# Kernel tuning notes

Measured on AMD Instinct MI355X. Metric: run time of the kernel, lower is better.

The kernel has to match this reference:

```python
import jax, jax.numpy as jnp
import numpy as np

B, M, D, E, K, T = 8192, 6, 128, 5, 2, 60
SHARED_W, UNSHARED_W, LB_W = 0.3, 0.7, 0.01

def _gelu(x):
    return jax.nn.gelu(x, approximate=False)

def _mlp3(x, w1, b1, w2, b2, w3, b3):
    h = _gelu(x @ w1 + b1)
    h = _gelu(h @ w2 + b2)
    return h @ w3 + b3

def _expert_stack(x, w1, b1, w2, b2, w3, b3):
    # x: [N, D]; weights stacked over experts e -> grouped GEMMs
    h = _gelu(jnp.einsum('nd,edh->enh', x, w1) + b1[:, None, :])
    h = _gelu(jnp.einsum('enh,ehg->eng', h, w2) + b2[:, None, :])
    return jnp.einsum('eng,ego->eno', h, w3) + b3[:, None, :]

def setup_inputs():
    key = jax.random.key(0)
    ks = iter(jax.random.split(key, 64))
    p = lambda shape, s=0.05: s * jax.random.normal(next(ks), shape, dtype=jnp.float32)
    return {
        'mode_features': jax.random.normal(next(ks), (B, M, D), dtype=jnp.float32),
        'rw1': p((D, 256)), 'rb1': p((256,)), 'rw2': p((256, 128)), 'rb2': p((128,)),
        'rw3': p((128, E)), 'rb3': p((E,)),
        'sh_tw1': p((D, 256)), 'sh_tb1': p((256,)), 'sh_tw2': p((256, 256)), 'sh_tb2': p((256,)),
        'sh_tw3': p((256, T * 2)), 'sh_tb3': p((T * 2,)),
        'sh_sw1': p((D, 128)), 'sh_sb1': p((128,)), 'sh_sw2': p((128, 64)), 'sh_sb2': p((64,)),
        'sh_sw3': p((64, 1)), 'sh_sb3': p((1,)),
        'ex_tw1': p((E, D, 256)), 'ex_tb1': p((E, 256)), 'ex_tw2': p((E, 256, 256)), 'ex_tb2': p((E, 256)),
        'ex_tw3': p((E, 256, T * 2)), 'ex_tb3': p((E, T * 2)),
        'ex_sw1': p((E, D, 128)), 'ex_sb1': p((E, 128)), 'ex_sw2': p((E, 128, 64)), 'ex_sb2': p((E, 64)),
        'ex_sw3': p((E, 64, 1)), 'ex_sb3': p((E, 1)),
    }

def reference(mode_features, rw1, rb1, rw2, rb2, rw3, rb3,
              sh_tw1, sh_tb1, sh_tw2, sh_tb2, sh_tw3, sh_tb3,
              sh_sw1, sh_sb1, sh_sw2, sh_sb2, sh_sw3, sh_sb3,
              ex_tw1, ex_tb1, ex_tw2, ex_tb2, ex_tw3, ex_tb3,
              ex_sw1, ex_sb1, ex_sw2, ex_sb2, ex_sw3, ex_sb3):
    b, m, d = mode_features.shape
    x = mode_features.reshape(b * m, d)
    # router (Dropout is identity in eval mode)
    logits = _mlp3(x, rw1, rb1, rw2, rb2, rw3, rb3)                 # [N, E]
    probs = jax.nn.softmax(logits, axis=-1)
    router_logits = logits.reshape(b, m, E)
    topk_logits, topk_idx = jax.lax.top_k(router_logits, K)         # [B, M, K]
    topk_probs = jax.nn.softmax(topk_logits, axis=-1)
    # shared expert on all tokens
    shared_traj = _mlp3(x, sh_tw1, sh_tb1, sh_tw2, sh_tb2, sh_tw3, sh_tb3).reshape(b, m, T, 2)
    shared_score = _mlp3(x, sh_sw1, sh_sb1, sh_sw2, sh_sb2, sh_sw3, sh_sb3).reshape(b, m)
    # all unshared experts computed densely (torch code also computes these for expert_predictions)
    traj_all = _expert_stack(x, ex_tw1, ex_tb1, ex_tw2, ex_tb2, ex_tw3, ex_tb3).reshape(E, b, m, T, 2)
    score_all = _expert_stack(x, ex_sw1, ex_sb1, ex_sw2, ex_sb2, ex_sw3, ex_sb3).reshape(E, b, m)
    # top-k combine: gather selected expert outputs (same math as the torch dispatch + index_add_)
    traj_bme = jnp.transpose(traj_all, (1, 2, 0, 3, 4))             # [B, M, E, T, 2]
    score_bme = jnp.transpose(score_all, (1, 2, 0))                 # [B, M, E]
    idx5 = jnp.broadcast_to(topk_idx[..., None, None], (b, m, K, T, 2))
    sel_traj = jnp.take_along_axis(traj_bme, idx5, axis=2)          # [B, M, K, T, 2]
    sel_score = jnp.take_along_axis(score_bme, topk_idx, axis=2)    # [B, M, K]
    unshared_traj = jnp.einsum('bmktc,bmk->bmtc', sel_traj, topk_probs)
    unshared_score = jnp.sum(sel_score * topk_probs, axis=-1)
    final_traj = SHARED_W * shared_traj + UNSHARED_W * unshared_traj
    final_score = SHARED_W * shared_score + UNSHARED_W * unshared_score
    # load-balance aux loss
    avg_probs = jnp.mean(probs, axis=0)                             # [E]
    entropy = -jnp.sum(avg_probs * jnp.log(avg_probs + 1e-8))
    l2 = jnp.mean((avg_probs - 1.0 / E) ** 2)
    aux_loss = -entropy * LB_W + 0.01 * l2
    return (final_traj, final_score, router_logits, topk_idx, aux_loss, traj_all, score_all)
```

## Files before the change

### kernel.cpp

```cpp
#include <hip/hip_runtime.h>
#include <hip/hip_bf16.h>
#include <cstdint>
#include <cstddef>

static constexpr int N_TOK = 49152;
static constexpr size_t OFF_TRAJ     = 0;
static constexpr size_t OFF_SCORE    = 5898240;
static constexpr size_t OFF_LOGITS   = 5947392;
static constexpr size_t OFF_IDX      = 6193152;
static constexpr size_t OFF_AUX      = 6291456;
static constexpr size_t OFF_TRAJALL  = 6291457;
static constexpr size_t OFF_SCOREALL = 35782657;

typedef short s16x8 __attribute__((ext_vector_type(8)));
typedef float f32x4 __attribute__((ext_vector_type(4)));
typedef f32x4 f32x4u __attribute__((aligned(4)));
typedef unsigned int u32;
typedef unsigned short u16;

static constexpr u32 O_T1 = 0,      O_T2 = 196608, O_T3 = 589824;
static constexpr u32 O_S1 = 774144, O_S2 = 872448;
static constexpr u32 OB_T1 = 0, OB_T2 = 1536, OB_T3 = 3072, OB_S1 = 3792, OB_S2 = 4560;
static constexpr u32 OW_S3 = 4944, OB_S3 = 5328;

__device__ __forceinline__ float gelu_exact(float x) {
    return 0.5f * x * (1.0f + erff(x * 0.70710678118654752440f));
}
__device__ __forceinline__ float gelu_f(float x) {
    const float x2 = x * x;
    const float u  = x * fmaf(0.07135486172f, x2, 1.5957691216057308f);
    const float t  = __expf(-u);
    return x * __builtin_amdgcn_rcpf(1.0f + t);
}
__device__ __forceinline__ float bf2f(u16 u) {
    return __uint_as_float(((u32)u) << 16);
}
__device__ __forceinline__ u16 f2bf(float v) {
    return ((__hip_bfloat16_raw)__float2bfloat16(v)).x;
}
__device__ __forceinline__ void gload16(const u16* g, u16* l) {
    __builtin_amdgcn_global_load_lds(
        (const __attribute__((address_space(1))) u32*)g,
        (__attribute__((address_space(3))) u32*)l, 16, 0, 0);
}
#define MFMA16(a, b, c) __builtin_amdgcn_mfma_f32_16x16x32_bf16(a, b, c, 0, 0, 0)
#define SBAR() __builtin_amdgcn_sched_barrier(0)

__device__ __forceinline__ s16x8 lds_frag(const u16* buf, int RBu16, int r, int c) {
    return *(const s16x8*)&buf[r * RBu16 + ((c ^ (r & 7)) << 3)];
}
__device__ __forceinline__ void lds_store4(u16* buf, int RBu16, int r, int colb,
                                           float v0, float v1, float v2, float v3) {
    const int ch = (colb >> 3) ^ (r & 7);
    ushort4 st = { f2bf(v0), f2bf(v1), f2bf(v2), f2bf(v3) };
    *(ushort4*)&buf[r * RBu16 + ch * 8 + (colb & 7)] = st;
}

template<bool GELU>
__global__ __launch_bounds__(256)
void mlp_gemm(const float* __restrict__ A, const float* __restrict__ W,
              const float* __restrict__ bias, float* __restrict__ C,
              int Kd, int H)
{
    __shared__ float As[32][128];
    __shared__ float Ws[32][132];

    const int tid  = threadIdx.x;
    const int tx   = tid & 15;
    const int ty   = tid >> 4;
    const int row0 = blockIdx.x * 128;
    const int col0 = blockIdx.y * 128;
    const int lm = tid >> 1;
    const int lk = (tid & 1) * 16;

    float acc[8][8] = {};

    for (int k0 = 0; k0 < Kd; k0 += 32) {
        {
            const float* src = A + (size_t)(row0 + lm) * Kd + k0 + lk;
            #pragma unroll
            for (int q = 0; q < 4; ++q) {
                float4 f = *(const float4*)(src + q * 4);
                As[lk + q * 4 + 0][lm] = f.x;
                As[lk + q * 4 + 1][lm] = f.y;
                As[lk + q * 4 + 2][lm] = f.z;
                As[lk + q * 4 + 3][lm] = f.w;
            }
        }
        {
            #pragma unroll
            for (int q = 0; q < 2; ++q) {
                const float* wsrc = W + (size_t)(k0 + ty + q * 16) * H + col0 + tx * 8;
                float4 g0 = *(const float4*)wsrc;
                float4 g1 = *(const float4*)(wsrc + 4);
                *(float4*)&Ws[ty + q * 16][tx * 8]     = g0;
                *(float4*)&Ws[ty + q * 16][tx * 8 + 4] = g1;
            }
        }
        __syncthreads();
        #pragma unroll
        for (int kk = 0; kk < 32; ++kk) {
            float a[8], w[8];
            *(float4*)&a[0] = *(const float4*)&As[kk][ty * 8];
            *(float4*)&a[4] = *(const float4*)&As[kk][ty * 8 + 4];
            *(float4*)&w[0] = *(const float4*)&Ws[kk][tx * 8];
            *(float4*)&w[4] = *(const float4*)&Ws[kk][tx * 8 + 4];
            #pragma unroll
            for (int i = 0; i < 8; ++i)
                #pragma unroll
                for (int j = 0; j < 8; ++j)
                    acc[i][j] = fmaf(a[i], w[j], acc[i][j]);
        }
        __syncthreads();
    }

    #pragma unroll
    for (int i = 0; i < 8; ++i) {
        const int r = row0 + ty * 8 + i;
        #pragma unroll
        for (int j = 0; j < 8; ++j) {
            const int c = col0 + tx * 8 + j;
            float v = acc[i][j] + bias[c];
            if (GELU) v = gelu_exact(v);
            C[(size_t)r * H + c] = v;
        }
    }
}

__global__ __launch_bounds__(256)
void router_l3post(const float* __restrict__ rh2, const float* __restrict__ w3,
                   const float* __restrict__ b3, float* __restrict__ logits,
                   float* __restrict__ oidx, float* __restrict__ tp,
                   int* __restrict__ ti, float* __restrict__ part)
{
    __shared__ float w3s[640];
    __shared__ float red[256];
    const int tid = threadIdx.x;
    for (int i = tid; i < 640; i += 256) w3s[i] = w3[i];
    __syncthreads();

    const int n = blockIdx.x * 256 + tid;
    const float* h = rh2 + (size_t)n * 128;

    float l[5];
    #pragma unroll
    for (int e = 0; e < 5; ++e) l[e] = b3[e];
    for (int k = 0; k < 128; k += 4) {
        float4 hv = *(const float4*)(h + k);
        #pragma unroll
        for (int e = 0; e < 5; ++e) {
            l[e] = fmaf(hv.x, w3s[(k + 0) * 5 + e], l[e]);
            l[e] = fmaf(hv.y, w3s[(k + 1) * 5 + e], l[e]);
            l[e] = fmaf(hv.z, w3s[(k + 2) * 5 + e], l[e]);
            l[e] = fmaf(hv.w, w3s[(k + 3) * 5 + e], l[e]);
        }
    }
    #pragma unroll
    for (int e = 0; e < 5; ++e) logits[(size_t)n * 5 + e] = l[e];

    float m = l[0];
    #pragma unroll
    for (int e = 1; e < 5; ++e) m = fmaxf(m, l[e]);
    float p[5], s = 0.f;
    #pragma unroll
    for (int e = 0; e < 5; ++e) { p[e] = expf(l[e] - m); s += p[e]; }
    const float inv = 1.0f / s;

    #pragma unroll
    for (int e = 0; e < 5; ++e) {
        red[tid] = p[e] * inv;
        __syncthreads();
        for (int off = 128; off > 0; off >>= 1) {
            if (tid < off) red[tid] += red[tid + off];
            __syncthreads();
        }
        if (tid == 0) part[blockIdx.x * 5 + e] = red[0];
        __syncthreads();
    }

    int i0 = 0; float v0 = l[0];
    #pragma unroll
    for (int e = 1; e < 5; ++e) if (l[e] > v0) { v0 = l[e]; i0 = e; }
    int i1 = -1; float v1 = -1e30f;
    #pragma unroll
    for (int e = 0; e < 5; ++e) if (e != i0 && l[e] > v1) { v1 = l[e]; i1 = e; }

    const float t  = expf(v1 - v0);
    const float q0 = 1.0f / (1.0f + t);
    const float q1 = t / (1.0f + t);

    oidx[(size_t)n * 2]     = (float)i0;
    oidx[(size_t)n * 2 + 1] = (float)i1;
    tp[n * 2] = q0; tp[n * 2 + 1] = q1;
    ti[n * 2] = i0; ti[n * 2 + 1] = i1;
}

__global__ __launch_bounds__(256)
void aux_kernel(const float* __restrict__ part, float* __restrict__ aux)
{
    __shared__ float avg[5];
    const int tid = threadIdx.x;
    if (tid < 5) {
        float s = 0.f;
        for (int b = 0; b < 192; ++b) s += part[b * 5 + tid];
        avg[tid] = s / (float)N_TOK;
    }
    __syncthreads();
    if (tid == 0) {
        float ent = 0.f, l2 = 0.f;
        #pragma unroll
        for (int e = 0; e < 5; ++e) {
            ent -= avg[e] * logf(avg[e] + 1e-8f);
            float d = avg[e] - 0.2f;
            l2 += d * d;
        }
        l2 *= (1.0f / 5.0f);
        aux[0] = -ent * 0.01f + 0.01f * l2;
    }
}

__global__ __launch_bounds__(512, 2)
void expert_fused(const u16* __restrict__ xb, const u16* __restrict__ wtb,
                  const float* __restrict__ biasp, float* __restrict__ out,
                  float* __restrict__ shtraj, float* __restrict__ shscore)
{
    __shared__ u16 xs[64 * 128];
    __shared__ u16 hb[64 * 256];
    float* hbf = (float*)hb;
    u16* s1p = hb;
    u16* s2p = hb + 64 * 128;

    const int tid  = threadIdx.x;
    const int lane = tid & 63;
    const int wave = tid >> 6;
    const int row0 = blockIdx.x * 64;
    const int e    = blockIdx.y;
    const int frow = lane & 15;
    const int kgrp = lane >> 4;
    const int c0   = wave * 32;

    #pragma unroll
    for (int i = 0; i < 2; ++i) {
        const int idx = i * 512 + tid;
        const int r = idx >> 4, c = idx & 15;
        gload16(xb + (size_t)(row0 + r) * 128 + ((c ^ (r & 7)) << 3), &xs[idx * 8]);
    }

    const int col3 = wave * 16 + kgrp * 4;
    const int r3   = (wave * 16 + frow) < 120 ? (wave * 16 + frow) : 119;

    s16x8 wf1[4][2];
    {
        const u16* w1p = wtb + O_T1 + e * 32768;
        #pragma unroll
        for (int n = 0; n < 2; ++n) {
            const u16* p = w1p + (size_t)(c0 + n * 16 + frow) * 128 + kgrp * 8;
            #pragma unroll
            for (int ks = 0; ks < 4; ++ks) wf1[ks][n] = *(const s16x8*)(p + ks * 32);
        }
    }
    SBAR();

    __syncthreads();

    f32x4 acc1[4][2] = {};
    #pragma unroll
    for (int ks = 0; ks < 4; ++ks)
        #pragma unroll
        for (int m = 0; m < 4; ++m) {
            const s16x8 a = lds_frag(xs, 128, m * 16 + frow, ks * 4 + kgrp);
            #pragma unroll
            for (int n = 0; n < 2; ++n)
                acc1[m][n] = MFMA16(wf1[ks][n], a, acc1[m][n]);
        }

    const u16* w2p = wtb + O_T2 + e * 65536;
    s16x8 wf2a[4][2];
    f32x4 bb1[2];
    #pragma unroll
    for (int n = 0; n < 2; ++n) {
        const u16* p = w2p + (size_t)(c0 + n * 16 + frow) * 256 + kgrp * 8;
        #pragma unroll
        for (int ks = 0; ks < 4; ++ks) wf2a[ks][n] = *(const s16x8*)(p + ks * 32);
        bb1[n] = *(const f32x4*)&biasp[OB_T1 + e * 256 + c0 + n * 16 + kgrp * 4];
    }
    SBAR();

    {
        #pragma unroll
        for (int n = 0; n < 2; ++n) {
            const int colb = c0 + n * 16 + kgrp * 4;
            #pragma unroll
            for (int m = 0; m < 4; ++m)
                lds_store4(hb, 256, m * 16 + frow, colb,
                           gelu_f(acc1[m][n][0] + bb1[n][0]),
                           gelu_f(acc1[m][n][1] + bb1[n][1]),
                           gelu_f(acc1[m][n][2] + bb1[n][2]),
                           gelu_f(acc1[m][n][3] + bb1[n][3]));
        }
    }
    __syncthreads();

    s16x8 wf2b[4][2];
    #pragma unroll
    for (int n = 0; n < 2; ++n) {
        const u16* p = w2p + (size_t)(c0 + n * 16 + frow) * 256 + 128 + kgrp * 8;
        #pragma unroll
        for (int ks = 0; ks < 4; ++ks) wf2b[ks][n] = *(const s16x8*)(p + ks * 32);
    }
    SBAR();

    f32x4 acc2[4][2] = {};
    #pragma unroll
    for (int ks = 0; ks < 4; ++ks)
        #pragma unroll
        for (int m = 0; m < 4; ++m) {
            const s16x8 a = lds_frag(hb, 256, m * 16 + frow, ks * 4 + kgrp);
            #pragma unroll
            for (int n = 0; n < 2; ++n)
                acc2[m][n] = MFMA16(wf2a[ks][n], a, acc2[m][n]);
        }
    #pragma unroll
    for (int ks = 0; ks < 4; ++ks)
        #pragma unroll
        for (int m = 0; m < 4; ++m) {
            const s16x8 a = lds_frag(hb, 256, m * 16 + frow, (ks + 4) * 4 + kgrp);
            #pragma unroll
            for (int n = 0; n < 2; ++n)
                acc2[m][n] = MFMA16(wf2b[ks][n], a, acc2[m][n]);
        }

    s16x8 wf3[8];
    f32x4 bb2[2];
    {
        const u16* w3p = wtb + O_T3 + e * 30720 + (size_t)r3 * 256 + kgrp * 8;
        #pragma unroll
        for (int ks = 0; ks < 8; ++ks) wf3[ks] = *(const s16x8*)(w3p + ks * 32);
        #pragma unroll
        for (int n = 0; n < 2; ++n)
            bb2[n] = *(const f32x4*)&biasp[OB_T2 + e * 256 + c0 + n * 16 + kgrp * 4];
    }
    SBAR();
    __syncthreads();

    {
        #pragma unroll
        for (int n = 0; n < 2; ++n) {
            const int colb = c0 + n * 16 + kgrp * 4;
            #pragma unroll
            for (int m = 0; m < 4; ++m)
                lds_store4(hb, 256, m * 16 + frow, colb,
                           gelu_f(acc2[m][n][0] + bb2[n][0]),
                           gelu_f(acc2[m][n][1] + bb2[n][1]),
                           gelu_f(acc2[m][n][2] + bb2[n][2]),
                           gelu_f(acc2[m][n][3] + bb2[n][3]));
        }
    }
    __syncthreads();

    s16x8 wfs1[4];
    f32x4 bb3 = *(const f32x4u*)&biasp[OB_T3 + e * 120 + (col3 < 120 ? col3 : 116)];
    {
        const u16* p = wtb + O_S1 + e * 16384 + (size_t)(wave * 16 + frow) * 128 + kgrp * 8;
        #pragma unroll
        for (int ks = 0; ks < 4; ++ks) wfs1[ks] = *(const s16x8*)(p + ks * 32);
    }
    SBAR();

    f32x4 acc3[4] = {};
    #pragma unroll
    for (int ks = 0; ks < 8; ++ks)
        #pragma unroll
        for (int m = 0; m < 4; ++m) {
            const s16x8 a = lds_frag(hb, 256, m * 16 + frow, ks * 4 + kgrp);
            acc3[m] = MFMA16(wf3[ks], a, acc3[m]);
        }
    __syncthreads();

    f32x4 accs1[4] = {};
    #pragma unroll
    for (int ks = 0; ks < 4; ++ks)
        #pragma unroll
        for (int m = 0; m < 4; ++m) {
            const s16x8 a = lds_frag(xs, 128, m * 16 + frow, ks * 4 + kgrp);
            accs1[m] = MFMA16(wfs1[ks], a, accs1[m]);
        }
    s16x8 wfs2[4];
    f32x4 bbs1;
    {
        const u16* p = wtb + O_S2 + e * 8192 + (size_t)((wave & 3) * 16 + frow) * 128 + kgrp * 8;
        #pragma unroll
        for (int ks = 0; ks < 4; ++ks) wfs2[ks] = *(const s16x8*)(p + ks * 32);
        bbs1 = *(const f32x4*)&biasp[OB_S1 + e * 128 + wave * 16 + kgrp * 4];
    }
    SBAR();
    {
        const int colb = wave * 16 + kgrp * 4;
        #pragma unroll
        for (int m = 0; m < 4; ++m)
            lds_store4(s1p, 128, m * 16 + frow, colb,
                       gelu_f(accs1[m][0] + bbs1[0]),
                       gelu_f(accs1[m][1] + bbs1[1]),
                       gelu_f(accs1[m][2] + bbs1[2]),
                       gelu_f(accs1[m][3] + bbs1[3]));
    }
    __syncthreads();

    if (wave < 4) {
        f32x4 accs2[4] = {};
        #pragma unroll
        for (int ks = 0; ks < 4; ++ks)
            #pragma unroll
            for (int m = 0; m < 4; ++m) {
                const s16x8 a = lds_frag(s1p, 128, m * 16 + frow, ks * 4 + kgrp);
                accs2[m] = MFMA16(wfs2[ks], a, accs2[m]);
            }
        const int colb = wave * 16 + kgrp * 4;
        const f32x4 bb = *(const f32x4*)&biasp[OB_S2 + e * 64 + colb];
        #pragma unroll
        for (int m = 0; m < 4; ++m)
            lds_store4(s2p, 64, m * 16 + frow, colb,
                       gelu_f(accs2[m][0] + bb[0]),
                       gelu_f(accs2[m][1] + bb[1]),
                       gelu_f(accs2[m][2] + bb[2]),
                       gelu_f(accs2[m][3] + bb[3]));
    }
    __syncthreads();

    {
        const int tok = tid >> 3;
        const int kc  = tid & 7;
        const float* w3s = biasp + OW_S3 + e * 64 + kc * 8;
        const s16x8 v = lds_frag(s2p, 64, tok, kc);
        float p = 0.f;
        #pragma unroll
        for (int j = 0; j < 8; ++j) p = fmaf(bf2f((u16)v[j]), w3s[j], p);
        p += __shfl_xor(p, 1);
        p += __shfl_xor(p, 2);
        p += __shfl_xor(p, 4);
        if (kc == 0) {
            const float val = p + biasp[OB_S3 + e];
            if (e < 5) out[OFF_SCOREALL + (size_t)e * N_TOK + row0 + tok] = val;
            else       shscore[row0 + tok] = val;
        }
    }
    __syncthreads();

    if (col3 < 120) {
        #pragma unroll
        for (int m = 0; m < 4; ++m) {
            f32x4 v;
            #pragma unroll
            for (int j = 0; j < 4; ++j) v[j] = acc3[m][j] + bb3[j];
            *(f32x4*)&hbf[(m * 16 + frow) * 120 + col3] = v;
        }
    }
    __syncthreads();

    {
        float* dst = (e < 5) ? out + OFF_TRAJALL + ((size_t)e * N_TOK + row0) * 120
                             : shtraj + (size_t)row0 * 120;
        const int head = (int)((16 - (((size_t)dst) & 15)) & 15) >> 2;
        const int nvec = (7680 - head) >> 2;
        const int tail = 7680 - head - (nvec << 2);
        if (tid < head) dst[tid] = hbf[tid];
        if (tid >= 8 && tid < 8 + tail)
            dst[7680 - tail + (tid - 8)] = hbf[7680 - tail + (tid - 8)];
        #pragma unroll
        for (int i = 0; i < 4; ++i) {
            const int v = i * 512 + tid;
            if (v < nvec) {
                const int q = head + v * 4;
                f32x4 val;
                val[0] = hbf[q];     val[1] = hbf[q + 1];
                val[2] = hbf[q + 2]; val[3] = hbf[q + 3];
                *(f32x4*)(dst + q) = val;
            }
        }
    }
}

__global__ __launch_bounds__(256)
void combine_all(const float* __restrict__ trajall, const float* __restrict__ shtraj,
                 const float* __restrict__ scoreall, const float* __restrict__ shscore,
                 const float* __restrict__ tp, const int* __restrict__ ti,
                 float* __restrict__ ftraj, float* __restrict__ fscore)
{
    const int i4 = blockIdx.x * 256 + threadIdx.x;
    const int n  = i4 / 30;
    const int q4 = (i4 - n * 30) * 4;
    const int i0 = ti[n * 2], i1 = ti[n * 2 + 1];
    const float p0 = tp[n * 2], p1 = tp[n * 2 + 1];

    const f32x4 a = *(const f32x4u*)&trajall[((size_t)i0 * N_TOK + n) * 120 + q4];
    const f32x4 b = *(const f32x4u*)&trajall[((size_t)i1 * N_TOK + n) * 120 + q4];
    const f32x4 s = *(const f32x4*)&shtraj[(size_t)n * 120 + q4];
    f32x4 r;
    #pragma unroll
    for (int j = 0; j < 4; ++j)
        r[j] = 0.3f * s[j] + 0.7f * (p0 * a[j] + p1 * b[j]);
    *(f32x4*)&ftraj[(size_t)n * 120 + q4] = r;

    if (q4 == 0) {
        const float sa = scoreall[(size_t)i0 * N_TOK + n];
        const float sb = scoreall[(size_t)i1 * N_TOK + n];
        fscore[n] = 0.3f * shscore[n] + 0.7f * (p0 * sa + p1 * sb);
    }
}

__global__ __launch_bounds__(256)
void convert_x(const float* __restrict__ x, u16* __restrict__ xb)
{
    const size_t i = ((size_t)blockIdx.x * 256 + threadIdx.x) * 4;
    float4 v = *(const float4*)(x + i);
    ushort4 o;
    o.x = f2bf(v.x); o.y = f2bf(v.y); o.z = f2bf(v.z); o.w = f2bf(v.w);
    *(ushort4*)(xb + i) = o;
}

struct WDesc { const float* src; u32 dstOff; int K, H, nz; };
struct WTable { WDesc d[10]; };

__global__ __launch_bounds__(256)
void convert_w(WTable t, u16* __restrict__ dst)
{
    const WDesc dd = t.d[blockIdx.y];
    const int tilesK = dd.K >> 5;
    const int tilesH = (dd.H + 31) >> 5;
    const int tt = blockIdx.x;
    if (tt >= tilesK * tilesH * dd.nz) return;
    const int e  = tt / (tilesK * tilesH);
    const int r  = tt - e * (tilesK * tilesH);
    const int th = r / tilesK;
    const int tk = r - th * tilesK;

    __shared__ float tile[32][33];
    const int tx = threadIdx.x & 31;
    const int ty = threadIdx.x >> 5;

    #pragma unroll
    for (int i = 0; i < 4; ++i) {
        const int k = tk * 32 + ty + i * 8;
        const int h = th * 32 + tx;
        tile[ty + i * 8][tx] = (h < dd.H)
            ? dd.src[((size_t)e * dd.K + k) * dd.H + h] : 0.0f;
    }
    __syncthreads();
    #pragma unroll
    for (int i = 0; i < 4; ++i) {
        const int h = th * 32 + ty + i * 8;
        const int k = tk * 32 + tx;
        if (h < dd.H)
            dst[dd.dstOff + ((size_t)e * dd.H + h) * dd.K + k] = f2bf(tile[tx][ty + i * 8]);
    }
}

struct CDesc { const float* src; u32 dstOff; u32 n; };
struct CTable { CDesc d[14]; };

__global__ __launch_bounds__(256)
void pack_f32(CTable t, float* __restrict__ dst)
{
    const CDesc dd = t.d[blockIdx.y];
    const u32 i = blockIdx.x * 256 + threadIdx.x;
    if (i < dd.n) dst[dd.dstOff + i] = dd.src[i];
}

extern "C" void kernel_launch(void* const* d_in, const int* in_sizes, int n_in,
                              void* d_out, int out_size, void* d_ws, size_t ws_size,
                              hipStream_t stream)
{
    (void)in_sizes; (void)n_in; (void)out_size; (void)ws_size;

    const float* x   = (const float*)d_in[0];
    const float* rw1 = (const float*)d_in[1];
    const float* rb1 = (const float*)d_in[2];
    const float* rw2 = (const float*)d_in[3];
    const float* rb2 = (const float*)d_in[4];
    const float* rw3 = (const float*)d_in[5];
    const float* rb3 = (const float*)d_in[6];

    float* out = (float*)d_out;
    char* ws = (char*)d_ws;

    u16*   xb      = (u16*)(ws);
    u16*   wtb     = (u16*)(ws + 12582912);
    float* biasp   = (float*)(ws + 14426112);
    float* part    = (float*)(ws + 14447616);
    float* tp      = (float*)(ws + 14451712);
    int*   ti      = (int*)  (ws + 14844928);
    float* shscore = (float*)(ws + 15238144);
    float* shtraj  = (float*)(ws + 15434752);
    float* rh1     = (float*)(ws + 39027712);
    float* rh2     = (float*)(ws + 89359360);

    const dim3 blk(256);

    mlp_gemm<true ><<<dim3(N_TOK / 128, 2), blk, 0, stream>>>(x,   rw1, rb1, rh1, 128, 256);
    mlp_gemm<true ><<<dim3(N_TOK / 128, 1), blk, 0, stream>>>(rh1, rw2, rb2, rh2, 256, 128);
    router_l3post<<<dim3(N_TOK / 256), blk, 0, stream>>>(
        rh2, rw3, rb3, out + OFF_LOGITS, out + OFF_IDX, tp, ti, part);
    aux_kernel<<<dim3(1), blk, 0, stream>>>(part, out + OFF_AUX);

    convert_x<<<dim3(N_TOK * 128 / 1024), blk, 0, stream>>>(x, xb);
    {
        WTable t;
        t.d[0] = { (const float*)d_in[19], O_T1,              128, 256, 5 };
        t.d[1] = { (const float*)d_in[7],  O_T1 + 5 * 32768,  128, 256, 1 };
        t.d[2] = { (const float*)d_in[21], O_T2,              256, 256, 5 };
        t.d[3] = { (const float*)d_in[9],  O_T2 + 5 * 65536,  256, 256, 1 };
        t.d[4] = { (const float*)d_in[23], O_T3,              256, 120, 5 };
        t.d[5] = { (const float*)d_in[11], O_T3 + 5 * 30720,  256, 120, 1 };
        t.d[6] = { (const float*)d_in[25], O_S1,              128, 128, 5 };
        t.d[7] = { (const float*)d_in[13], O_S1 + 5 * 16384,  128, 128, 1 };
        t.d[8] = { (const float*)d_in[27], O_S2,              128,  64, 5 };
        t.d[9] = { (const float*)d_in[15], O_S2 + 5 * 8192,   128,  64, 1 };
        convert_w<<<dim3(320, 10), blk, 0, stream>>>(t, wtb);
    }
    {
        CTable t;
        t.d[0]  = { (const float*)d_in[20], OB_T1,        1280 };
        t.d[1]  = { (const float*)d_in[8],  OB_T1 + 1280,  256 };
        t.d[2]  = { (const float*)d_in[22], OB_T2,        1280 };
        t.d[3]  = { (const float*)d_in[10], OB_T2 + 1280,  256 };
        t.d[4]  = { (const float*)d_in[24], OB_T3,         600 };
        t.d[5]  = { (const float*)d_in[12], OB_T3 + 600,   120 };
        t.d[6]  = { (const float*)d_in[26], OB_S1,         640 };
        t.d[7]  = { (const float*)d_in[14], OB_S1 + 640,   128 };
        t.d[8]  = { (const float*)d_in[28], OB_S2,         320 };
        t.d[9]  = { (const float*)d_in[16], OB_S2 + 320,    64 };
        t.d[10] = { (const float*)d_in[29], OW_S3,         320 };
        t.d[11] = { (const float*)d_in[17], OW_S3 + 320,    64 };
        t.d[12] = { (const float*)d_in[30], OB_S3,           5 };
        t.d[13] = { (const float*)d_in[18], OB_S3 + 5,       1 };
        pack_f32<<<dim3(5, 14), blk, 0, stream>>>(t, biasp);
    }

    expert_fused<<<dim3(N_TOK / 64, 6), dim3(512), 0, stream>>>(
        xb, wtb, biasp, out, shtraj, shscore);

    combine_all<<<dim3(N_TOK * 30 / 256), blk, 0, stream>>>(
        out + OFF_TRAJALL, shtraj, out + OFF_SCOREALL, shscore,
        tp, ti, out + OFF_TRAJ, out + OFF_SCORE);
}
```

Measured before the change: 391.1 us.

## Fuse router MLP, top-k, softmax partials and x bf16 conversion into one kernel

Replaces the two tiled fp32 router GEMM kernels, the layer-3/top-k kernel and the separate x-to-bf16 conversion with a single kernel. Each 512-thread block handles 32 tokens and keeps the hidden activations in LDS, so the rh1/rh2 intermediates never go to global memory. The aux kernel now reduces 1536 partials instead of 192. The expert kernel's staging buffer is also padded to a row stride of 124, likely to cut LDS bank conflicts, at the cost of index divisions in the copy-out. Each block re-streams the full router weights through LDS and uses a small per-thread register tile on scalar FMAs, which may give lower FMA efficiency than the previous 8x8 tiles.

Result: slower. 416.3 us (+6.5%).

```diff
diff --git a/kernel.cpp b/kernel.cpp
--- a/kernel.cpp
+++ b/kernel.cpp
@@ -56,143 +56,166 @@
     *(ushort4*)&buf[r * RBu16 + ch * 8 + (colb & 7)] = st;
 }
 
-template<bool GELU>
-__global__ __launch_bounds__(256)
-void mlp_gemm(const float* __restrict__ A, const float* __restrict__ W,
-              const float* __restrict__ bias, float* __restrict__ C,
-              int Kd, int H)
+__global__ __launch_bounds__(512, 2)
+void router_fused(const float* __restrict__ x, const float* __restrict__ rw1,
+                  const float* __restrict__ rb1, const float* __restrict__ rw2,
+                  const float* __restrict__ rb2, const float* __restrict__ rw3,
+                  const float* __restrict__ rb3, u16* __restrict__ xb,
+                  float* __restrict__ logits, float* __restrict__ oidx,
+                  float* __restrict__ tp, int* __restrict__ ti,
+                  float* __restrict__ part)
 {
-    __shared__ float As[32][128];
-    __shared__ float Ws[32][132];
+    __shared__ float bufA[32 * 128];
+    __shared__ float bufB[32 * 256];
+    __shared__ float bufC[32 * 256];
 
     const int tid  = threadIdx.x;
-    const int tx   = tid & 15;
-    const int ty   = tid >> 4;
-    const int row0 = blockIdx.x * 128;
-    const int col0 = blockIdx.y * 128;
-    const int lm = tid >> 1;
-    const int lk = (tid & 1) * 16;
-
-    float acc[8][8] = {};
-
-    for (int k0 = 0; k0 < Kd; k0 += 32) {
-        {
-            const float* src = A + (size_t)(row0 + lm) * Kd + k0 + lk;
-            #pragma unroll
-            for (int q = 0; q < 4; ++q) {
-                float4 f = *(const float4*)(src + q * 4);
-                As[lk + q * 4 + 0][lm] = f.x;
-                As[lk + q * 4 + 1][lm] = f.y;
-                As[lk + q * 4 + 2][lm] = f.z;
-                As[lk + q * 4 + 3][lm] = f.w;
+    const int row0 = blockIdx.x * 32;
+    const int tg   = tid >> 6;
+    const int cl   = tid & 63;
+    const int t0   = tg * 4;
+
+    {
+        const float* src = x + (size_t)row0 * 128;
+        #pragma unroll
+        for (int i = 0; i < 2; ++i)
+            *(float4*)&bufA[i * 2048 + tid * 4] = *(const float4*)&src[i * 2048 + tid * 4];
+    }
+    __syncthreads();
+
+    {
+        u16* dst = xb + (size_t)row0 * 128;
+        const int base = tid * 8;
+        ushort4 o0, o1;
+        o0.x = f2bf(bufA[base + 0]); o0.y = f2bf(bufA[base + 1]);
+        o0.z = f2bf(bufA[base + 2]); o0.w = f2bf(bufA[base + 3]);
+        o1.x = f2bf(bufA[base + 4]); o1.y = f2bf(bufA[base + 5]);
+        o1.z = f2bf(bufA[base + 6]); o1.w = f2bf(bufA[base + 7]);
+        *(ushort4*)&dst[base]     = o0;
+        *(ushort4*)&dst[base + 4] = o1;
+    }
+
+    float acc1[4][4] = {};
+    for (int k0 = 0; k0 < 128; k0 += 32) {
+        __syncthreads();
+        #pragma unroll
+        for (int i = 0; i < 4; ++i)
+            *(float4*)&bufB[i * 2048 + tid * 4] =
+                *(const float4*)&rw1[(size_t)k0 * 256 + i * 2048 + tid * 4];
+        __syncthreads();
+        #pragma unroll
+        for (int kk = 0; kk < 32; ++kk) {
+            const float4 wv = *(const float4*)&bufB[kk * 256 + cl * 4];
+            #pragma unroll
+            for (int i = 0; i < 4; ++i) {
+                const float xv = bufA[(t0 + i) * 128 + k0 + kk];
+                acc1[i][0] = fmaf(xv, wv.x, acc1[i][0]);
+                acc1[i][1] = fmaf(xv, wv.y, acc1[i][1]);
+                acc1[i][2] = fmaf(xv, wv.z, acc1[i][2]);
+                acc1[i][3] = fmaf(xv, wv.w, acc1[i][3]);
             }
         }
-        {
-            #pragma unroll
-            for (int q = 0; q < 2; ++q) {
-                const float* wsrc = W + (size_t)(k0 + ty + q * 16) * H + col0 + tx * 8;
-                float4 g0 = *(const float4*)wsrc;
-                float4 g1 = *(const float4*)(wsrc + 4);
-                *(float4*)&Ws[ty + q * 16][tx * 8]     = g0;
-                *(float4*)&Ws[ty + q * 16][tx * 8 + 4] = g1;
+    }
+    {
+        const float4 b1 = *(const float4*)&rb1[cl * 4];
+        #pragma unroll
+        for (int i = 0; i < 4; ++i) {
+            bufC[(t0 + i) * 256 + cl * 4 + 0] = gelu_exact(acc1[i][0] + b1.x);
+            bufC[(t0 + i) * 256 + cl * 4 + 1] = gelu_exact(acc1[i][1] + b1.y);
+            bufC[(t0 + i) * 256 + cl * 4 + 2] = gelu_exact(acc1[i][2] + b1.z);
+            bufC[(t0 + i) * 256 + cl * 4 + 3] = gelu_exact(acc1[i][3] + b1.w);
+        }
+    }
+    __syncthreads();
+
+    float acc2[4][2] = {};
+    for (int k0 = 0; k0 < 256; k0 += 32) {
+        __syncthreads();
+        #pragma unroll
+        for (int i = 0; i < 2; ++i)
+            *(float4*)&bufA[i * 2048 + tid * 4] =
+                *(const float4*)&rw2[(size_t)k0 * 128 + i * 2048 + tid * 4];
+        __syncthreads();
+        #pragma unroll
+        for (int kk = 0; kk < 32; ++kk) {
+            const float2 wv = *(const float2*)&bufA[kk * 128 + cl * 2];
+            #pragma unroll
+            for (int i = 0; i < 4; ++i) {
+                const float hv = bufC[(t0 + i) * 256 + k0 + kk];
+                acc2[i][0] = fmaf(hv, wv.x, acc2[i][0]);
+                acc2[i][1] = fmaf(hv, wv.y, acc2[i][1]);
             }
         }
-        __syncthreads();
-        #pragma unroll
-        for (int kk = 0; kk < 32; ++kk) {
-            float a[8], w[8];
-            *(float4*)&a[0] = *(const float4*)&As[kk][ty * 8];
-            *(float4*)&a[4] = *(const float4*)&As[kk][ty * 8 + 4];
-            *(float4*)&w[0] = *(const float4*)&Ws[kk][tx * 8];
-            *(float4*)&w[4] = *(const float4*)&Ws[kk][tx * 8 + 4];
-            #pragma unroll
-            for (int i = 0; i < 8; ++i)
-                #pragma unroll
-                for (int j = 0; j < 8; ++j)
-                    acc[i][j] = fmaf(a[i], w[j], acc[i][j]);
-        }
-        __syncthreads();
-    }
-
-    #pragma unroll
-    for (int i = 0; i < 8; ++i) {
-        const int r = row0 + ty * 8 + i;
-        #pragma unroll
-        for (int j = 0; j < 8; ++j) {
-            const int c = col0 + tx * 8 + j;
-            float v = acc[i][j] + bias[c];
-            if (GELU) v = gelu_exact(v);
-            C[(size_t)r * H + c] = v;
-        }
-    }
-}
-
-__global__ __launch_bounds__(256)
-void router_l3post(const float* __restrict__ rh2, const float* __restrict__ w3,
-                   const float* __restrict__ b3, float* __restrict__ logits,
-                   float* __restrict__ oidx, float* __restrict__ tp,
-                   int* __restrict__ ti, float* __restrict__ part)
-{
-    __shared__ float w3s[640];
-    __shared__ float red[256];
-    const int tid = threadIdx.x;
-    for (int i = tid; i < 640; i += 256) w3s[i] = w3[i];
-    __syncthreads();
-
-    const int n = blockIdx.x * 256 + tid;
-    const float* h = rh2 + (size_t)n * 128;
-
-    float l[5];
-    #pragma unroll
-    for (int e = 0; e < 5; ++e) l[e] = b3[e];
-    for (int k = 0; k < 128; k += 4) {
-        float4 hv = *(const float4*)(h + k);
-        #pragma unroll
-        for (int e = 0; e < 5; ++e) {
-            l[e] = fmaf(hv.x, w3s[(k + 0) * 5 + e], l[e]);
-            l[e] = fmaf(hv.y, w3s[(k + 1) * 5 + e], l[e]);
-            l[e] = fmaf(hv.z, w3s[(k + 2) * 5 + e], l[e]);
-            l[e] = fmaf(hv.w, w3s[(k + 3) * 5 + e], l[e]);
-        }
-    }
-    #pragma unroll
-    for (int e = 0; e < 5; ++e) logits[(size_t)n * 5 + e] = l[e];
-
-    float m = l[0];
-    #pragma unroll
-    for (int e = 1; e < 5; ++e) m = fmaxf(m, l[e]);
-    float p[5], s = 0.f;
-    #pragma unroll
-    for (int e = 0; e < 5; ++e) { p[e] = expf(l[e] - m); s += p[e]; }
-    const float inv = 1.0f / s;
-
-    #pragma unroll
-    for (int e = 0; e < 5; ++e) {
-        red[tid] = p[e] * inv;
-        __syncthreads();
-        for (int off = 128; off > 0; off >>= 1) {
-            if (tid < off) red[tid] += red[tid + off];
-            __syncthreads();
-        }
-        if (tid == 0) part[blockIdx.x * 5 + e] = red[0];
-        __syncthreads();
-    }
-
-    int i0 = 0; float v0 = l[0];
-    #pragma unroll
-    for (int e = 1; e < 5; ++e) if (l[e] > v0) { v0 = l[e]; i0 = e; }
-    int i1 = -1; float v1 = -1e30f;
-    #pragma unroll
-    for (int e = 0; e < 5; ++e) if (e != i0 && l[e] > v1) { v1 = l[e]; i1 = e; }
-
-    const float t  = expf(v1 - v0);
-    const float q0 = 1.0f / (1.0f + t);
-    const float q1 = t / (1.0f + t);
-
-    oidx[(size_t)n * 2]     = (float)i0;
-    oidx[(size_t)n * 2 + 1] = (float)i1;
-    tp[n * 2] = q0; tp[n * 2 + 1] = q1;
-    ti[n * 2] = i0; ti[n * 2 + 1] = i1;
+    }
+    {
+        const float2 b2 = *(const float2*)&rb2[cl * 2];
+        #pragma unroll
+        for (int i = 0; i < 4; ++i) {
+            bufB[(t0 + i) * 128 + cl * 2 + 0] = gelu_exact(acc2[i][0] + b2.x);
+            bufB[(t0 + i) * 128 + cl * 2 + 1] = gelu_exact(acc2[i][1] + b2.y);
+        }
+    }
+    __syncthreads();
+
+    {
+        const int tok = tid >> 4;
+        const int ln  = tid & 15;
+        float l5[5] = {0.f, 0.f, 0.f, 0.f, 0.f};
+        #pragma unroll
+        for (int kk = 0; kk < 8; ++kk) {
+            const float hv = bufB[tok * 128 + ln * 8 + kk];
+            #pragma unroll
+            for (int e = 0; e < 5; ++e)
+                l5[e] = fmaf(hv, rw3[(size_t)(ln * 8 + kk) * 5 + e], l5[e]);
+        }
+        #pragma unroll
+        for (int off = 8; off > 0; off >>= 1)
+            #pragma unroll
+            for (int e = 0; e < 5; ++e)
+                l5[e] += __shfl_xor(l5[e], off);
+
+        if (ln == 0) {
+            const int n = row0 + tok;
+            float l[5];
+            #pragma unroll
+            for (int e = 0; e < 5; ++e) {
+                l[e] = l5[e] + rb3[e];
+                logits[(size_t)n * 5 + e] = l[e];
+            }
+            float m = l[0];
+            #pragma unroll
+            for (int e = 1; e < 5; ++e) m = fmaxf(m, l[e]);
+            float p[5], s = 0.f;
+            #pragma unroll
+            for (int e = 0; e < 5; ++e) { p[e] = expf(l[e] - m); s += p[e]; }
+            const float inv = 1.0f / s;
+            #pragma unroll
+            for (int e = 0; e < 5; ++e) bufC[tok * 5 + e] = p[e] * inv;
+
+            int i0 = 0; float v0 = l[0];
+            #pragma unroll
+            for (int e = 1; e < 5; ++e) if (l[e] > v0) { v0 = l[e]; i0 = e; }
+            int i1 = -1; float v1 = -1e30f;
+            #pragma unroll
+            for (int e = 0; e < 5; ++e) if (e != i0 && l[e] > v1) { v1 = l[e]; i1 = e; }
+
+            const float t  = expf(v1 - v0);
+            const float q0 = 1.0f / (1.0f + t);
+            const float q1 = t / (1.0f + t);
+
+            oidx[(size_t)n * 2]     = (float)i0;
+            oidx[(size_t)n * 2 + 1] = (float)i1;
+            tp[n * 2] = q0; tp[n * 2 + 1] = q1;
+            ti[n * 2] = i0; ti[n * 2 + 1] = i1;
+        }
+    }
+    __syncthreads();
+    if (tid < 5) {
+        float s = 0.f;
+        #pragma unroll 8
+        for (int t = 0; t < 32; ++t) s += bufC[t * 5 + tid];
+        part[blockIdx.x * 5 + tid] = s;
+    }
 }
 
 __global__ __launch_bounds__(256)
@@ -202,7 +225,7 @@
     const int tid = threadIdx.x;
     if (tid < 5) {
         float s = 0.f;
-        for (int b = 0; b < 192; ++b) s += part[b * 5 + tid];
+        for (int b = 0; b < 1536; ++b) s += part[b * 5 + tid];
         avg[tid] = s / (float)N_TOK;
     }
     __syncthreads();
@@ -452,7 +475,7 @@
             f32x4 v;
             #pragma unroll
             for (int j = 0; j < 4; ++j) v[j] = acc3[m][j] + bb3[j];
-            *(f32x4*)&hbf[(m * 16 + frow) * 120 + col3] = v;
+            *(f32x4*)&hbf[(m * 16 + frow) * 124 + col3] = v;
         }
     }
     __syncthreads();
@@ -463,17 +486,29 @@
         const int head = (int)((16 - (((size_t)dst) & 15)) & 15) >> 2;
         const int nvec = (7680 - head) >> 2;
         const int tail = 7680 - head - (nvec << 2);
-        if (tid < head) dst[tid] = hbf[tid];
-        if (tid >= 8 && tid < 8 + tail)
-            dst[7680 - tail + (tid - 8)] = hbf[7680 - tail + (tid - 8)];
+        if (tid < head) {
+            const int t0i = tid;
+            dst[t0i] = hbf[(t0i / 120) * 124 + (t0i % 120)];
+        }
+        if (tid >= 8 && tid < 8 + tail) {
+            const int t0i = 7680 - tail + (tid - 8);
+            dst[t0i] = hbf[(t0i / 120) * 124 + (t0i % 120)];
+        }
         #pragma unroll
         for (int i = 0; i < 4; ++i) {
             const int v = i * 512 + tid;
             if (v < nvec) {
                 const int q = head + v * 4;
+                const int tok = q / 120;
+                const int colq = q - tok * 120;
                 f32x4 val;
-                val[0] = hbf[q];     val[1] = hbf[q + 1];
-                val[2] = hbf[q + 2]; val[3] = hbf[q + 3];
+                #pragma unroll
+                for (int j = 0; j < 4; ++j) {
+                    const int qq = q + j;
+                    const int tk = qq / 120;
+                    val[j] = hbf[tk * 124 + (qq - tk * 120)];
+                }
+                (void)tok; (void)colq;
                 *(f32x4*)(dst + q) = val;
             }
         }
@@ -506,16 +541,6 @@
         const float sb = scoreall[(size_t)i1 * N_TOK + n];
         fscore[n] = 0.3f * shscore[n] + 0.7f * (p0 * sa + p1 * sb);
     }
-}
-
-__global__ __launch_bounds__(256)
-void convert_x(const float* __restrict__ x, u16* __restrict__ xb)
-{
-    const size_t i = ((size_t)blockIdx.x * 256 + threadIdx.x) * 4;
-    float4 v = *(const float4*)(x + i);
-    ushort4 o;
-    o.x = f2bf(v.x); o.y = f2bf(v.y); o.z = f2bf(v.z); o.w = f2bf(v.w);
-    *(ushort4*)(xb + i) = o;
 }
 
 struct WDesc { const float* src; u32 dstOff; int K, H, nz; };
@@ -587,22 +612,18 @@
     u16*   wtb     = (u16*)(ws + 12582912);
     float* biasp   = (float*)(ws + 14426112);
     float* part    = (float*)(ws + 14447616);
-    float* tp      = (float*)(ws + 14451712);
-    int*   ti      = (int*)  (ws + 14844928);
-    float* shscore = (float*)(ws + 15238144);
-    float* shtraj  = (float*)(ws + 15434752);
-    float* rh1     = (float*)(ws + 39027712);
-    float* rh2     = (float*)(ws + 89359360);
+    float* tp      = (float*)(ws + 14478336);
+    int*   ti      = (int*)  (ws + 14871552);
+    float* shscore = (float*)(ws + 15264768);
+    float* shtraj  = (float*)(ws + 15461376);
 
     const dim3 blk(256);
 
-    mlp_gemm<true ><<<dim3(N_TOK / 128, 2), blk, 0, stream>>>(x,   rw1, rb1, rh1, 128, 256);
-    mlp_gemm<true ><<<dim3(N_TOK / 128, 1), blk, 0, stream>>>(rh1, rw2, rb2, rh2, 256, 128);
-    router_l3post<<<dim3(N_TOK / 256), blk, 0, stream>>>(
-        rh2, rw3, rb3, out + OFF_LOGITS, out + OFF_IDX, tp, ti, part);
+    router_fused<<<dim3(N_TOK / 32), dim3(512), 0, stream>>>(
+        x, rw1, rb1, rw2, rb2, rw3, rb3, xb,
+        out + OFF_LOGITS, out + OFF_IDX, tp, ti, part);
     aux_kernel<<<dim3(1), blk, 0, stream>>>(part, out + OFF_AUX);
 
-    convert_x<<<dim3(N_TOK * 128 / 1024), blk, 0, stream>>>(x, xb);
     {
         WTable t;
         t.d[0] = { (const float*)d_in[19], O_T1,              128, 256, 5 };
```
